# Optimization experiments

Measured on AMD Instinct MI355X. Metric: run time of the kernel, lower is better.

Reference implementation:

```python
import jax, jax.numpy as jnp
import numpy as np

B, L, D = 64, 512, 768
KSIZE, PAD = 3, 1
BN_EPS = 1e-5
COS_EPS = 1e-8

def _gauss_kernel(kernel_size, sigma, k):
    X = np.linspace(-k, k, kernel_size)
    x, y = np.meshgrid(X, X)
    g = 1.0 / (2 * np.pi * sigma ** 2) * np.exp(-(x ** 2 + y ** 2) / (2 * sigma ** 2))
    return g.astype(np.float32)

def setup_inputs() -> dict:
    key = jax.random.key(0)
    k1, k2, k3, k4 = jax.random.split(key, 4)
    news = jax.random.normal(k1, (B, L, D), dtype=jnp.float32)
    post = jax.random.normal(k2, (B, L, D), dtype=jnp.float32)
    gauss_kernel = jnp.asarray(_gauss_kernel(KSIZE, 2, 1))[None, None]  # (1,1,3,3), frozen
    bn_gamma = jnp.ones((1,), jnp.float32)
    bn_beta = jnp.zeros((1,), jnp.float32)
    bound = 1.0 / np.sqrt(L)
    lin_w = jax.random.uniform(k3, (L, L), jnp.float32, -bound, bound)
    lin_b = jax.random.uniform(k4, (L,), jnp.float32, -bound, bound)
    return {"news": news, "post": post, "gauss_kernel": gauss_kernel,
            "bn_gamma": bn_gamma, "bn_beta": bn_beta, "lin_w": lin_w, "lin_b": lin_b}

def reference(news, post, gauss_kernel, bn_gamma, bn_beta, lin_w, lin_b):
    # cosine similarity along feature dim (torch eps semantics)
    nn_ = jnp.maximum(jnp.linalg.norm(news, axis=-1), COS_EPS)
    np_ = jnp.maximum(jnp.linalg.norm(post, axis=-1), COS_EPS)
    cos = jnp.sum(news * post, axis=-1) / (nn_ * np_)           # (B, L)
    # the original loop writes the same cos row into every i -> broadcast
    trans = jnp.broadcast_to(cos[:, None, :], (cos.shape[0], cos.shape[1], cos.shape[1]))
    x = trans[:, None]                                           # (B,1,L,L)
    wk = jax.lax.conv_general_dilated(
        x, gauss_kernel, window_strides=(1, 1),
        padding=[(PAD, PAD), (PAD, PAD)],
        dimension_numbers=("NCHW", "OIHW", "NCHW"))             # (B,1,L,L)
    # BatchNorm2d(1) in training mode: batch stats over (N,H,W)
    mu = jnp.mean(wk)
    var = jnp.mean((wk - mu) ** 2)
    wk = (wk - mu) * jax.lax.rsqrt(var + BN_EPS) * bn_gamma[0] + bn_beta[0]
    wk = wk[:, 0]                                                # (B,L,L)
    wk = jnp.einsum("blm,nm->bln", wk, lin_w) + lin_b            # Linear over last dim
    wk = jax.nn.softmax(wk, axis=-2).sum(axis=-1)[..., None]     # (B,L,1)
    word_feat = (wk * news).mean(axis=1)                         # (B,D)
    post_feat = (wk * post).mean(axis=1)[:, None]                # (B,1,D)
    return (word_feat, post_feat)
```

## Files before the change

### kernel.cpp

```cpp
#include <hip/hip_runtime.h>
#include <math.h>

#define NB 64
#define NL 512
#define ND 768

static constexpr float kCosEps = 1e-8f;
static constexpr double kBnEps = 1e-5;

static constexpr size_t OFF_ACC = 0;
static constexpr size_t OFF_CSN = 256;
static constexpr size_t SZ_CS   = (size_t)NB * ND * 4;
static constexpr size_t OFF_CSP = OFF_CSN + SZ_CS;
static constexpr size_t MEMSET_BYTES = OFF_CSP + SZ_CS;
static constexpr size_t OFF_COS = 393728;
static constexpr size_t SZ_BL   = (size_t)NB * NL * 4;
static constexpr size_t OFF_HI  = OFF_COS + SZ_BL;
static constexpr size_t OFF_HT  = OFF_HI + SZ_BL;
static constexpr size_t OFF_HB  = OFF_HT + SZ_BL;
static constexpr size_t OFF_ABC = OFF_HB + SZ_BL;

__device__ __forceinline__ float dot4(float4 a, float4 b) {
    return a.x * b.x + a.y * b.y + a.z * b.z + a.w * b.w;
}

#define GLD16(ldst, gsrc)                                                        \
    __builtin_amdgcn_global_load_lds(                                            \
        (const __attribute__((address_space(1))) void*)(gsrc),                   \
        (__attribute__((address_space(3))) void*)(ldst), 16, 0, 0)

__global__ __launch_bounds__(256) void k1_cos_colsum(
    const float* __restrict__ news, const float* __restrict__ post,
    float* __restrict__ cosv, float* __restrict__ csn,
    float* __restrict__ csp)
{
    __shared__ float stage[2][8 * ND];
    const int b    = blockIdx.x >> 4;
    const int t16  = blockIdx.x & 15;
    const int l0   = t16 * 32;
    const int tid  = threadIdx.x;
    const int wave = tid >> 6;
    const int lane = tid & 63;

    const float* nbase = news + ((size_t)b * NL + l0 + wave) * ND + lane * 4;
    const float* pbase = post + ((size_t)b * NL + l0 + wave) * ND + lane * 4;

    float nn[8], pp[8], npd[8];
    float an[12], ap[12];
#pragma unroll
    for (int k = 0; k < 12; ++k) { an[k] = 0.f; ap[k] = 0.f; }

#pragma unroll
    for (int k = 0; k < 3; ++k) {
        GLD16(&stage[0][wave * ND + k * 256],       nbase + k * 256);
        GLD16(&stage[0][(4 + wave) * ND + k * 256], pbase + k * 256);
    }
    __syncthreads();

    for (int c = 0; c < 8; ++c) {
        const int cur = c & 1;
        if (c < 7) {
            const int nxt = cur ^ 1;
            const size_t goff = (size_t)(c + 1) * 4 * ND;
#pragma unroll
            for (int k = 0; k < 3; ++k) {
                GLD16(&stage[nxt][wave * ND + k * 256],       nbase + goff + k * 256);
                GLD16(&stage[nxt][(4 + wave) * ND + k * 256], pbase + goff + k * 256);
            }
        }
        const float4* ln = (const float4*)&stage[cur][wave * ND];
        const float4* lp = (const float4*)&stage[cur][(4 + wave) * ND];
        const float4 A0 = ln[lane], A1 = ln[lane + 64], A2 = ln[lane + 128];
        const float4 B0 = lp[lane], B1 = lp[lane + 64], B2 = lp[lane + 128];

        nn[c]  = dot4(A0, A0) + dot4(A1, A1) + dot4(A2, A2);
        pp[c]  = dot4(B0, B0) + dot4(B1, B1) + dot4(B2, B2);
        npd[c] = dot4(A0, B0) + dot4(A1, B1) + dot4(A2, B2);

        an[0] += A0.x; an[1] += A0.y; an[2]  += A0.z; an[3]  += A0.w;
        an[4] += A1.x; an[5] += A1.y; an[6]  += A1.z; an[7]  += A1.w;
        an[8] += A2.x; an[9] += A2.y; an[10] += A2.z; an[11] += A2.w;
        ap[0] += B0.x; ap[1] += B0.y; ap[2]  += B0.z; ap[3]  += B0.w;
        ap[4] += B1.x; ap[5] += B1.y; ap[6]  += B1.z; ap[7]  += B1.w;
        ap[8] += B2.x; ap[9] += B2.y; ap[10] += B2.z; ap[11] += B2.w;

        __syncthreads();
    }

#pragma unroll
    for (int m = 1; m <= 32; m <<= 1) {
#pragma unroll
        for (int c = 0; c < 8; ++c) {
            nn[c]  += __shfl_xor(nn[c], m);
            pp[c]  += __shfl_xor(pp[c], m);
            npd[c] += __shfl_xor(npd[c], m);
        }
    }
    if (lane == 0) {
#pragma unroll
        for (int c = 0; c < 8; ++c) {
            const float dn = fmaxf(sqrtf(nn[c]), kCosEps) * fmaxf(sqrtf(pp[c]), kCosEps);
            cosv[b * NL + l0 + c * 4 + wave] = npd[c] / dn;
        }
    }

    {
        float4* wn = (float4*)&stage[0][wave * ND];
        float4* wp = (float4*)&stage[0][(4 + wave) * ND];
        wn[lane]       = make_float4(an[0], an[1], an[2], an[3]);
        wn[lane + 64]  = make_float4(an[4], an[5], an[6], an[7]);
        wn[lane + 128] = make_float4(an[8], an[9], an[10], an[11]);
        wp[lane]       = make_float4(ap[0], ap[1], ap[2], ap[3]);
        wp[lane + 64]  = make_float4(ap[4], ap[5], ap[6], ap[7]);
        wp[lane + 128] = make_float4(ap[8], ap[9], ap[10], ap[11]);
    }
    __syncthreads();
    for (int i = tid; i < ND; i += 256) {
        float sn = 0.f, sp = 0.f;
#pragma unroll
        for (int w = 0; w < 4; ++w) {
            sn += stage[0][w * ND + i];
            sp += stage[0][(4 + w) * ND + i];
        }
        atomicAdd(&csn[b * ND + i], sn);
        atomicAdd(&csp[b * ND + i], sp);
    }
}

__global__ __launch_bounds__(256) void k2_conv_stats(
    const float* __restrict__ cosv, const float* __restrict__ g,
    float* __restrict__ hi, float* __restrict__ ht, float* __restrict__ hb,
    double* __restrict__ acc)
{
    __shared__ float row[NL + 2];
    __shared__ double sred[8];
    const int b   = blockIdx.x;
    const int tid = threadIdx.x;
    if (tid == 0) { row[0] = 0.f; row[NL + 1] = 0.f; }
    for (int j = tid; j < NL; j += 256) row[j + 1] = cosv[b * NL + j];
    __syncthreads();

    const float ci0 = g[0] + g[3] + g[6], ci1 = g[1] + g[4] + g[7], ci2 = g[2] + g[5] + g[8];
    const float ct0 = g[3] + g[6],        ct1 = g[4] + g[7],        ct2 = g[5] + g[8];
    const float cb0 = g[0] + g[3],        cb1 = g[1] + g[4],        cb2 = g[2] + g[5];

    double s = 0.0, s2 = 0.0;
    for (int j = tid; j < NL; j += 256) {
        const float a = row[j], c = row[j + 1], d = row[j + 2];
        const float vi = ci0 * a + ci1 * c + ci2 * d;
        const float vt = ct0 * a + ct1 * c + ct2 * d;
        const float vb = cb0 * a + cb1 * c + cb2 * d;
        hi[b * NL + j] = vi; ht[b * NL + j] = vt; hb[b * NL + j] = vb;
        s  += (double)vi * (NL - 2) + (double)vt + (double)vb;
        s2 += (double)vi * vi * (NL - 2) + (double)vt * vt + (double)vb * vb;
    }
    const int lane = tid & 63, wave = tid >> 6;
#pragma unroll
    for (int m = 32; m >= 1; m >>= 1) { s += __shfl_xor(s, m); s2 += __shfl_xor(s2, m); }
    if (lane == 0) { sred[wave] = s; sred[4 + wave] = s2; }
    __syncthreads();
    if (tid == 0) {
        atomicAdd(&acc[0], sred[0] + sred[1] + sred[2] + sred[3]);
        atomicAdd(&acc[1], sred[4] + sred[5] + sred[6] + sred[7]);
    }
}

__global__ __launch_bounds__(256) void k3_linear_softmax(
    const float* __restrict__ hi, const float* __restrict__ ht,
    const float* __restrict__ hb, const float* __restrict__ W,
    const float* __restrict__ bias, const float* __restrict__ gamma,
    const float* __restrict__ beta, const double* __restrict__ acc,
    float* __restrict__ abc)
{
    __shared__ float shi[NL], sht[NL], shb[NL];
    __shared__ float sred[12];
    const int b   = blockIdx.x;
    const int tid = threadIdx.x;

    const double N   = (double)NB * NL * NL;
    const double mu  = acc[0] / N;
    const double var = acc[1] / N - mu * mu;
    const float  sc  = gamma[0] * (float)(1.0 / sqrt(var + kBnEps));
    const float  sh  = beta[0] - (float)mu * sc;

    for (int j = tid; j < NL; j += 256) {
        shi[j] = hi[b * NL + j] * sc + sh;
        sht[j] = ht[b * NL + j] * sc + sh;
        shb[j] = hb[b * NL + j] * sc + sh;
    }
    __syncthreads();

    const float4* s4i = (const float4*)shi;
    const float4* s4t = (const float4*)sht;
    const float4* s4b = (const float4*)shb;

    float sa = 0.f, st = 0.f, sb = 0.f;
    for (int n = tid; n < NL; n += 256) {
        const float4* wr = (const float4*)(W + (size_t)n * NL);
        float zi = 0.f, zt = 0.f, zb = 0.f;
        for (int m = 0; m < NL / 4; ++m) {
            const float4 w  = wr[m];
            const float4 vi = s4i[m], vt = s4t[m], vb = s4b[m];
            zi += w.x * vi.x + w.y * vi.y + w.z * vi.z + w.w * vi.w;
            zt += w.x * vt.x + w.y * vt.y + w.z * vt.z + w.w * vt.w;
            zb += w.x * vb.x + w.y * vb.y + w.z * vb.z + w.w * vb.w;
        }
        const float bv = bias[n];
        zi += bv; zt += bv; zb += bv;
        const float M  = fmaxf(zi, fmaxf(zt, zb));
        const float ei = expf(zi - M), et = expf(zt - M), eb = expf(zb - M);
        const float r  = 1.f / ((float)(NL - 2) * ei + et + eb);
        sa += ei * r; st += et * r; sb += eb * r;
    }
    const int lane = tid & 63, wave = tid >> 6;
#pragma unroll
    for (int m = 32; m >= 1; m >>= 1) {
        sa += __shfl_xor(sa, m); st += __shfl_xor(st, m); sb += __shfl_xor(sb, m);
    }
    if (lane == 0) { sred[wave * 3] = sa; sred[wave * 3 + 1] = st; sred[wave * 3 + 2] = sb; }
    __syncthreads();
    if (tid == 0) {
        abc[b * 3 + 0] = sred[0] + sred[3] + sred[6] + sred[9];
        abc[b * 3 + 1] = sred[1] + sred[4] + sred[7] + sred[10];
        abc[b * 3 + 2] = sred[2] + sred[5] + sred[8] + sred[11];
    }
}

__global__ __launch_bounds__(256) void k4_out(
    const float* __restrict__ news, const float* __restrict__ post,
    const float* __restrict__ csn, const float* __restrict__ csp,
    const float* __restrict__ abc, float* __restrict__ out)
{
    const int idx = blockIdx.x * 256 + threadIdx.x;
    if (idx >= NB * ND) return;
    const int b = idx / ND, d = idx - b * ND;
    const float a  = abc[b * 3 + 0];
    const float ct = abc[b * 3 + 1];
    const float cb = abc[b * 3 + 2];
    const float cn = csn[idx];
    const float cp = csp[idx];
    const size_t base = (size_t)b * NL * ND;
    const float n0 = news[base + d], nL = news[base + (size_t)(NL - 1) * ND + d];
    const float p0 = post[base + d], pL = post[base + (size_t)(NL - 1) * ND + d];
    const float invL = 1.f / NL;
    out[idx]           = (a * cn + (ct - a) * n0 + (cb - a) * nL) * invL;
    out[NB * ND + idx] = (a * cp + (ct - a) * p0 + (cb - a) * pL) * invL;
}

extern "C" void kernel_launch(void* const* d_in, const int* in_sizes, int n_in,
                              void* d_out, int out_size, void* d_ws, size_t ws_size,
                              hipStream_t stream) {
    const float* news     = (const float*)d_in[0];
    const float* post     = (const float*)d_in[1];
    const float* g        = (const float*)d_in[2];
    const float* bn_gamma = (const float*)d_in[3];
    const float* bn_beta  = (const float*)d_in[4];
    const float* lin_w    = (const float*)d_in[5];
    const float* lin_b    = (const float*)d_in[6];
    float* out = (float*)d_out;
    char*  ws  = (char*)d_ws;

    double* acc = (double*)(ws + OFF_ACC);
    float* csn  = (float*)(ws + OFF_CSN);
    float* csp  = (float*)(ws + OFF_CSP);
    float* cosv = (float*)(ws + OFF_COS);
    float* hi   = (float*)(ws + OFF_HI);
    float* ht   = (float*)(ws + OFF_HT);
    float* hb   = (float*)(ws + OFF_HB);
    float* abc  = (float*)(ws + OFF_ABC);

    hipMemsetAsync(ws, 0, MEMSET_BYTES, stream);

    k1_cos_colsum<<<NB * 16, 256, 0, stream>>>(news, post, cosv, csn, csp);
    k2_conv_stats<<<NB, 256, 0, stream>>>(cosv, g, hi, ht, hb, acc);
    k3_linear_softmax<<<NB, 256, 0, stream>>>(hi, ht, hb, lin_w, lin_b,
                                              bn_gamma, bn_beta, acc, abc);
    k4_out<<<192, 256, 0, stream>>>(news, post, csn, csp, abc, out);
}
```

Before: 91.75 us.

## Give each wave private contiguous rows and replace block barriers with vmcnt waits

Each wave now streams its own 8 contiguous rows of news and post through a per-wave double buffer in LDS, instead of interleaving rows across the four waves. Because no wave reads another wave's staging, the per-chunk __syncthreads is replaced by s_waitcnt vmcnt on that wave's own async global-to-LDS loads. This removes block-wide barrier stalls in the streaming loop and lets waves drift independently. It depends on the vmcnt count matching the number of outstanding async LDS loads per lane, and on the wave's own LDS writes being visible to its reads once vmcnt drains.

```diff
diff --git a/kernel.cpp b/kernel.cpp
--- a/kernel.cpp
+++ b/kernel.cpp
@@ -29,12 +29,18 @@
         (const __attribute__((address_space(1))) void*)(gsrc),                   \
         (__attribute__((address_space(3))) void*)(ldst), 16, 0, 0)
 
+#define WAIT_VMCNT(n)                                                            \
+    do {                                                                         \
+        asm volatile("s_waitcnt vmcnt(" #n ")" ::: "memory");                    \
+        __builtin_amdgcn_sched_barrier(0);                                       \
+    } while (0)
+
 __global__ __launch_bounds__(256) void k1_cos_colsum(
     const float* __restrict__ news, const float* __restrict__ post,
     float* __restrict__ cosv, float* __restrict__ csn,
     float* __restrict__ csp)
 {
-    __shared__ float stage[2][8 * ND];
+    __shared__ float ring[2][4][2][ND];
     const int b    = blockIdx.x >> 4;
     const int t16  = blockIdx.x & 15;
     const int l0   = t16 * 32;
@@ -42,8 +48,8 @@
     const int wave = tid >> 6;
     const int lane = tid & 63;
 
-    const float* nbase = news + ((size_t)b * NL + l0 + wave) * ND + lane * 4;
-    const float* pbase = post + ((size_t)b * NL + l0 + wave) * ND + lane * 4;
+    const float* nbase = news + ((size_t)b * NL + l0 + wave * 8) * ND + lane * 4;
+    const float* pbase = post + ((size_t)b * NL + l0 + wave * 8) * ND + lane * 4;
 
     float nn[8], pp[8], npd[8];
     float an[12], ap[12];
@@ -52,24 +58,27 @@
 
 #pragma unroll
     for (int k = 0; k < 3; ++k) {
-        GLD16(&stage[0][wave * ND + k * 256],       nbase + k * 256);
-        GLD16(&stage[0][(4 + wave) * ND + k * 256], pbase + k * 256);
-    }
-    __syncthreads();
+        GLD16(&ring[0][wave][0][k * 256], nbase + k * 256);
+        GLD16(&ring[0][wave][1][k * 256], pbase + k * 256);
+    }
 
     for (int c = 0; c < 8; ++c) {
         const int cur = c & 1;
         if (c < 7) {
             const int nxt = cur ^ 1;
-            const size_t goff = (size_t)(c + 1) * 4 * ND;
+            const size_t go = (size_t)(c + 1) * ND;
 #pragma unroll
             for (int k = 0; k < 3; ++k) {
-                GLD16(&stage[nxt][wave * ND + k * 256],       nbase + goff + k * 256);
-                GLD16(&stage[nxt][(4 + wave) * ND + k * 256], pbase + goff + k * 256);
+                GLD16(&ring[nxt][wave][0][k * 256], nbase + go + k * 256);
+                GLD16(&ring[nxt][wave][1][k * 256], pbase + go + k * 256);
             }
-        }
-        const float4* ln = (const float4*)&stage[cur][wave * ND];
-        const float4* lp = (const float4*)&stage[cur][(4 + wave) * ND];
+            WAIT_VMCNT(6);
+        } else {
+            WAIT_VMCNT(0);
+        }
+
+        const float4* ln = (const float4*)&ring[cur][wave][0][0];
+        const float4* lp = (const float4*)&ring[cur][wave][1][0];
         const float4 A0 = ln[lane], A1 = ln[lane + 64], A2 = ln[lane + 128];
         const float4 B0 = lp[lane], B1 = lp[lane + 64], B2 = lp[lane + 128];
 
@@ -83,8 +92,6 @@
         ap[0] += B0.x; ap[1] += B0.y; ap[2]  += B0.z; ap[3]  += B0.w;
         ap[4] += B1.x; ap[5] += B1.y; ap[6]  += B1.z; ap[7]  += B1.w;
         ap[8] += B2.x; ap[9] += B2.y; ap[10] += B2.z; ap[11] += B2.w;
-
-        __syncthreads();
     }
 
 #pragma unroll
@@ -100,13 +107,15 @@
 #pragma unroll
         for (int c = 0; c < 8; ++c) {
             const float dn = fmaxf(sqrtf(nn[c]), kCosEps) * fmaxf(sqrtf(pp[c]), kCosEps);
-            cosv[b * NL + l0 + c * 4 + wave] = npd[c] / dn;
-        }
-    }
-
+            cosv[b * NL + l0 + wave * 8 + c] = npd[c] / dn;
+        }
+    }
+
+    __syncthreads();
+    float* fb = &ring[0][0][0][0];
     {
-        float4* wn = (float4*)&stage[0][wave * ND];
-        float4* wp = (float4*)&stage[0][(4 + wave) * ND];
+        float4* wn = (float4*)&fb[wave * ND];
+        float4* wp = (float4*)&fb[(4 + wave) * ND];
         wn[lane]       = make_float4(an[0], an[1], an[2], an[3]);
         wn[lane + 64]  = make_float4(an[4], an[5], an[6], an[7]);
         wn[lane + 128] = make_float4(an[8], an[9], an[10], an[11]);
@@ -119,8 +128,8 @@
         float sn = 0.f, sp = 0.f;
 #pragma unroll
         for (int w = 0; w < 4; ++w) {
-            sn += stage[0][w * ND + i];
-            sp += stage[0][(4 + w) * ND + i];
+            sn += fb[w * ND + i];
+            sp += fb[(4 + w) * ND + i];
         }
         atomicAdd(&csn[b * ND + i], sn);
         atomicAdd(&csp[b * ND + i], sp);
```

New measurement: 97.14 us. 1.06x slower.

## Replace LDS double-buffered staging in cosine kernel with direct register loads

Applied to the files above, without the earlier changes.

The cosine/column-sum kernel no longer stages rows through LDS using global_load_lds with a double buffer and per-chunk barriers. Each wave now loads its 4 rows of news and post straight into registers in one burst, and the grid doubles to 2048 blocks of 16 rows each. This removes the LDS round trip and the synchronisations and exposes more memory-level parallelism. In exchange it uses more registers and issues twice as many atomicAdds on the column sums.

```diff
diff --git a/kernel.cpp b/kernel.cpp
--- a/kernel.cpp
+++ b/kernel.cpp
@@ -24,89 +24,73 @@
     return a.x * b.x + a.y * b.y + a.z * b.z + a.w * b.w;
 }
 
-#define GLD16(ldst, gsrc)                                                        \
-    __builtin_amdgcn_global_load_lds(                                            \
-        (const __attribute__((address_space(1))) void*)(gsrc),                   \
-        (__attribute__((address_space(3))) void*)(ldst), 16, 0, 0)
-
 __global__ __launch_bounds__(256) void k1_cos_colsum(
     const float* __restrict__ news, const float* __restrict__ post,
     float* __restrict__ cosv, float* __restrict__ csn,
     float* __restrict__ csp)
 {
-    __shared__ float stage[2][8 * ND];
-    const int b    = blockIdx.x >> 4;
-    const int t16  = blockIdx.x & 15;
-    const int l0   = t16 * 32;
+    __shared__ float red[8][ND];
+    const int b    = blockIdx.x >> 5;
+    const int t    = blockIdx.x & 31;
+    const int l0   = t * 16;
     const int tid  = threadIdx.x;
     const int wave = tid >> 6;
     const int lane = tid & 63;
 
-    const float* nbase = news + ((size_t)b * NL + l0 + wave) * ND + lane * 4;
-    const float* pbase = post + ((size_t)b * NL + l0 + wave) * ND + lane * 4;
-
-    float nn[8], pp[8], npd[8];
+    const size_t rbase = ((size_t)b * NL + l0 + wave * 4) * ND;
+    const float4* nr = (const float4*)(news + rbase) + lane;
+    const float4* pr = (const float4*)(post + rbase) + lane;
+
+    float4 N[4][3], P[4][3];
+#pragma unroll
+    for (int r = 0; r < 4; ++r)
+#pragma unroll
+        for (int k = 0; k < 3; ++k)
+            N[r][k] = nr[r * 192 + k * 64];
+#pragma unroll
+    for (int r = 0; r < 4; ++r)
+#pragma unroll
+        for (int k = 0; k < 3; ++k)
+            P[r][k] = pr[r * 192 + k * 64];
+
+    float nn[4], pp[4], npd[4];
     float an[12], ap[12];
 #pragma unroll
     for (int k = 0; k < 12; ++k) { an[k] = 0.f; ap[k] = 0.f; }
-
-#pragma unroll
-    for (int k = 0; k < 3; ++k) {
-        GLD16(&stage[0][wave * ND + k * 256],       nbase + k * 256);
-        GLD16(&stage[0][(4 + wave) * ND + k * 256], pbase + k * 256);
-    }
-    __syncthreads();
-
-    for (int c = 0; c < 8; ++c) {
-        const int cur = c & 1;
-        if (c < 7) {
-            const int nxt = cur ^ 1;
-            const size_t goff = (size_t)(c + 1) * 4 * ND;
-#pragma unroll
-            for (int k = 0; k < 3; ++k) {
-                GLD16(&stage[nxt][wave * ND + k * 256],       nbase + goff + k * 256);
-                GLD16(&stage[nxt][(4 + wave) * ND + k * 256], pbase + goff + k * 256);
-            }
-        }
-        const float4* ln = (const float4*)&stage[cur][wave * ND];
-        const float4* lp = (const float4*)&stage[cur][(4 + wave) * ND];
-        const float4 A0 = ln[lane], A1 = ln[lane + 64], A2 = ln[lane + 128];
-        const float4 B0 = lp[lane], B1 = lp[lane + 64], B2 = lp[lane + 128];
-
-        nn[c]  = dot4(A0, A0) + dot4(A1, A1) + dot4(A2, A2);
-        pp[c]  = dot4(B0, B0) + dot4(B1, B1) + dot4(B2, B2);
-        npd[c] = dot4(A0, B0) + dot4(A1, B1) + dot4(A2, B2);
-
-        an[0] += A0.x; an[1] += A0.y; an[2]  += A0.z; an[3]  += A0.w;
-        an[4] += A1.x; an[5] += A1.y; an[6]  += A1.z; an[7]  += A1.w;
-        an[8] += A2.x; an[9] += A2.y; an[10] += A2.z; an[11] += A2.w;
-        ap[0] += B0.x; ap[1] += B0.y; ap[2]  += B0.z; ap[3]  += B0.w;
-        ap[4] += B1.x; ap[5] += B1.y; ap[6]  += B1.z; ap[7]  += B1.w;
-        ap[8] += B2.x; ap[9] += B2.y; ap[10] += B2.z; ap[11] += B2.w;
-
-        __syncthreads();
+#pragma unroll
+    for (int r = 0; r < 4; ++r) {
+        nn[r]  = dot4(N[r][0], N[r][0]) + dot4(N[r][1], N[r][1]) + dot4(N[r][2], N[r][2]);
+        pp[r]  = dot4(P[r][0], P[r][0]) + dot4(P[r][1], P[r][1]) + dot4(P[r][2], P[r][2]);
+        npd[r] = dot4(N[r][0], P[r][0]) + dot4(N[r][1], P[r][1]) + dot4(N[r][2], P[r][2]);
+#pragma unroll
+        for (int k = 0; k < 3; ++k) {
+            an[4 * k + 0] += N[r][k].x; an[4 * k + 1] += N[r][k].y;
+            an[4 * k + 2] += N[r][k].z; an[4 * k + 3] += N[r][k].w;
+            ap[4 * k + 0] += P[r][k].x; ap[4 * k + 1] += P[r][k].y;
+            ap[4 * k + 2] += P[r][k].z; ap[4 * k + 3] += P[r][k].w;
+        }
     }
 
 #pragma unroll
     for (int m = 1; m <= 32; m <<= 1) {
 #pragma unroll
-        for (int c = 0; c < 8; ++c) {
-            nn[c]  += __shfl_xor(nn[c], m);
-            pp[c]  += __shfl_xor(pp[c], m);
-            npd[c] += __shfl_xor(npd[c], m);
+        for (int r = 0; r < 4; ++r) {
+            nn[r]  += __shfl_xor(nn[r], m);
+            pp[r]  += __shfl_xor(pp[r], m);
+            npd[r] += __shfl_xor(npd[r], m);
         }
     }
     if (lane == 0) {
 #pragma unroll
-        for (int c = 0; c < 8; ++c) {
-            const float dn = fmaxf(sqrtf(nn[c]), kCosEps) * fmaxf(sqrtf(pp[c]), kCosEps);
-            cosv[b * NL + l0 + c * 4 + wave] = npd[c] / dn;
+        for (int r = 0; r < 4; ++r) {
+            const float dn = fmaxf(sqrtf(nn[r]), kCosEps) * fmaxf(sqrtf(pp[r]), kCosEps);
+            cosv[b * NL + l0 + wave * 4 + r] = npd[r] / dn;
         }
     }
 
     {
-        float4* wn = (float4*)&stage[0][wave * ND];
-        float4* wp = (float4*)&stage[0][(4 + wave) * ND];
+        float4* wn = (float4*)&red[wave][0];
+        float4* wp = (float4*)&red[4 + wave][0];
         wn[lane]       = make_float4(an[0], an[1], an[2], an[3]);
         wn[lane + 64]  = make_float4(an[4], an[5], an[6], an[7]);
         wn[lane + 128] = make_float4(an[8], an[9], an[10], an[11]);
@@ -116,12 +100,8 @@
     }
     __syncthreads();
     for (int i = tid; i < ND; i += 256) {
-        float sn = 0.f, sp = 0.f;
-#pragma unroll
-        for (int w = 0; w < 4; ++w) {
-            sn += stage[0][w * ND + i];
-            sp += stage[0][(4 + w) * ND + i];
-        }
+        float sn = red[0][i] + red[1][i] + red[2][i] + red[3][i];
+        float sp = red[4][i] + red[5][i] + red[6][i] + red[7][i];
         atomicAdd(&csn[b * ND + i], sn);
         atomicAdd(&csp[b * ND + i], sp);
     }
@@ -271,7 +251,7 @@
 
     hipMemsetAsync(ws, 0, MEMSET_BYTES, stream);
 
-    k1_cos_colsum<<<NB * 16, 256, 0, stream>>>(news, post, cosv, csn, csp);
+    k1_cos_colsum<<<NB * 32, 256, 0, stream>>>(news, post, cosv, csn, csp);
     k2_conv_stats<<<NB, 256, 0, stream>>>(cosv, g, hi, ht, hb, acc);
     k3_linear_softmax<<<NB, 256, 0, stream>>>(hi, ht, hb, lin_w, lin_b,
                                               bn_gamma, bn_beta, acc, abc);
```

Result: faster. 87.81 us (-4.3%).
